# Optimization experiments

Measured on AMD Instinct MI355X. Metric: run time of the kernel, lower is better.

Reference implementation:

```python
import jax, jax.numpy as jnp
import numpy as np

N_NODES = 100000
D = 128
N_EDGES = 500000
HIDDEN = 256
NUM_CLASSES = 32


def setup_inputs() -> dict:
    key = jax.random.key(0)
    k0, k1, k2, k3 = jax.random.split(key, 4)
    node_embeddings = jax.random.normal(k0, (N_NODES, D), dtype=jnp.float32)
    edge_index = jax.random.randint(k1, (2, N_EDGES), 0, N_NODES, dtype=jnp.int64)
    # Linear weights in torch layout: [out_features, in_features]
    W1 = jax.random.normal(k2, (HIDDEN, 2 * D), dtype=jnp.float32) * (1.0 / np.sqrt(2 * D))
    b1 = jnp.zeros((HIDDEN,), dtype=jnp.float32)
    W2 = jax.random.normal(k3, (NUM_CLASSES, HIDDEN), dtype=jnp.float32) * (1.0 / np.sqrt(HIDDEN))
    b2 = jnp.zeros((NUM_CLASSES,), dtype=jnp.float32)
    return {"node_embeddings": node_embeddings, "edge_index": edge_index,
            "W1": W1, "b1": b1, "W2": W2, "b2": b2}


def reference(node_embeddings, edge_index, W1, b1, W2, b2):
    h = node_embeddings[edge_index[0]]            # [E, D]
    t = node_embeddings[edge_index[1]]            # [E, D]
    edge_emb = jnp.concatenate([h, t], axis=1)    # [E, 2D]
    out = edge_emb @ W1.T + b1                    # [E, HIDDEN]
    out = jax.nn.relu(out)
    out = out @ W2.T + b2                         # [E, NUM_CLASSES]
    return out
```

## Files before the change

kernel.cpp:

```cpp
#include <hip/hip_runtime.h>

constexpr int D    = 128;
constexpr int K2   = 256;
constexpr int H    = 256;
constexpr int CLS  = 32;
constexpr int MT   = 64;
constexpr int LSTR = 264;

typedef __attribute__((ext_vector_type(8))) __bf16 bf16x8;
typedef __attribute__((ext_vector_type(8))) unsigned short ushort8;
typedef __attribute__((ext_vector_type(4))) float f32x4;

static __device__ __forceinline__ unsigned short f2b(float f) {
  unsigned int u = __float_as_uint(f);
  u += 0x7FFFu + ((u >> 16) & 1u);
  return (unsigned short)(u >> 16);
}

static __device__ __forceinline__ void gld_lds16(const unsigned short* gp, unsigned short* lp) {
  __builtin_amdgcn_global_load_lds(
      (const __attribute__((address_space(1))) void*)gp,
      (__attribute__((address_space(3))) void*)lp, 16, 0, 0);
}

__global__ void prep_weights(const float* __restrict__ W1, const float* __restrict__ W2,
                             const void* __restrict__ eidx,
                             unsigned short* __restrict__ W1b, unsigned short* __restrict__ W2b,
                             unsigned short* __restrict__ W2s,
                             int* __restrict__ flag64) {
  int i = blockIdx.x * 256 + threadIdx.x;
  if (i < H * K2)  W1b[i] = f2b(W1[i]);
  if (i < CLS * H) {
    unsigned short v = f2b(W2[i]);
    W2b[i] = v;
    int r = i >> 8, e = i & 255, g = e >> 3, j = e & 7;
    int slot = (g & 16) | ((g ^ (r & 15)) & 15);
    W2s[r * 256 + slot * 8 + j] = v;
  }
  if (blockIdx.x == 0 && threadIdx.x == 0) {
    const unsigned int* p = (const unsigned int*)eidx;
    int is64 = 1;
    for (int j = 0; j < 64; ++j) if (p[2 * j + 1] != 0u) { is64 = 0; break; }
    *flag64 = is64;
  }
}

__global__ void prep_table(const float* __restrict__ emb, unsigned short* __restrict__ tab, int n8) {
  int i = blockIdx.x * 256 + threadIdx.x;
  if (i < n8) {
    const float* gp = emb + (size_t)i * 8;
    f32x4 lo = *(const f32x4*)gp, hi = *(const f32x4*)(gp + 4);
    ushort8 v;
    v[0] = f2b(lo[0]); v[1] = f2b(lo[1]); v[2] = f2b(lo[2]); v[3] = f2b(lo[3]);
    v[4] = f2b(hi[0]); v[5] = f2b(hi[1]); v[6] = f2b(hi[2]); v[7] = f2b(hi[3]);
    *(ushort8*)(tab + (size_t)i * 8) = v;
  }
}

__global__ void prep_idx(const void* __restrict__ eidx, int* __restrict__ idx32, int n) {
  __shared__ int sflag;
  if (threadIdx.x == 0) {
    const unsigned int* p = (const unsigned int*)eidx;
    int is64 = 1;
    for (int j = 0; j < 64; ++j) if (p[2 * j + 1] != 0u) { is64 = 0; break; }
    sflag = is64;
  }
  __syncthreads();
  int j = blockIdx.x * 256 + threadIdx.x;
  if (j < n) idx32[j] = sflag ? (int)((const long long*)eidx)[j] : ((const int*)eidx)[j];
}

__global__ __launch_bounds__(256, 2)
void edge_mlp3(const unsigned short* __restrict__ tab, const int* __restrict__ idx32,
               const unsigned short* __restrict__ W1b, const unsigned short* __restrict__ W2s,
               const float* __restrict__ b1, const float* __restrict__ b2,
               float* __restrict__ out, int E, int ntiles) {
  __shared__ unsigned short Xs[2][MT * 256];
  __shared__ unsigned short W2l[CLS * 256];

  const int tid  = threadIdx.x;
  const int lane = tid & 63;
  const int w    = tid >> 6;
  const int l16  = lane & 15;
  const int q    = lane >> 4;

  bf16x8 afr[4][8];
  #pragma unroll
  for (int a = 0; a < 4; ++a) {
    const unsigned short* rp = W1b + (64 * w + 16 * a + l16) * K2 + q * 8;
    #pragma unroll
    for (int kk = 0; kk < 8; ++kk)
      afr[a][kk] = *(const bf16x8*)(rp + kk * 32);
  }
  f32x4 binit[4];
  #pragma unroll
  for (int a = 0; a < 4; ++a) binit[a] = *(const f32x4*)(b1 + 64 * w + 16 * a + 4 * q);
  f32x4 b2init[2];
  #pragma unroll
  for (int ct = 0; ct < 2; ++ct) b2init[ct] = *(const f32x4*)(b2 + 16 * ct + 4 * q);

  #pragma unroll
  for (int c = 0; c < 4; ++c) {
    const unsigned short* gp = W2s + (c * 256 + 64 * w + lane) * 8;
    unsigned short* lp = &W2l[(c * 256 + 64 * w) * 8];
    gld_lds16(gp, lp);
  }

  const int G    = lane & 31;
  const int half = G >> 4;
  const int sub  = lane >> 5;

  auto stage = [&](int t, int b) {
    #pragma unroll
    for (int c = 0; c < 8; ++c) {
      int mrow = 16 * w + 2 * c + sub;
      int e = t * MT + mrow; if (e >= E) e = E - 1;
      int id = idx32[half ? (E + e) : e];
      const unsigned short* gp = tab + (size_t)id * D + ((G ^ mrow) & 15) * 8;
      unsigned short* lp = &Xs[b][(16 * w + 2 * c) * 256];
      gld_lds16(gp, lp);
    }
  };

  int buf = 0;
  int t0 = blockIdx.x;
  if (t0 < ntiles) stage(t0, 0);
  asm volatile("s_waitcnt vmcnt(0)\n\ts_barrier" ::: "memory");

  for (int t = t0; t < ntiles; t += gridDim.x) {
    int tn = t + gridDim.x;
    if (tn < ntiles) stage(tn, buf ^ 1);
    __builtin_amdgcn_sched_barrier(0);

    f32x4 acc[4][4];
    #pragma unroll
    for (int a = 0; a < 4; ++a)
      #pragma unroll
      for (int tt = 0; tt < 4; ++tt) acc[a][tt] = binit[a];

    __builtin_amdgcn_s_setprio(1);
    #pragma unroll
    for (int tt = 0; tt < 4; ++tt) {
      const unsigned short* rowp = &Xs[buf][(16 * tt + l16) * 256];
      #pragma unroll
      for (int kk = 0; kk < 8; ++kk) {
        int slot = (4 * kk + q) ^ l16;
        bf16x8 bfrag = *(const bf16x8*)(rowp + slot * 8);
        #pragma unroll
        for (int a = 0; a < 4; ++a)
          acc[a][tt] = __builtin_amdgcn_mfma_f32_16x16x32_bf16(afr[a][kk], bfrag, acc[a][tt], 0, 0, 0);
      }
    }
    __builtin_amdgcn_s_setprio(0);
    asm volatile("s_barrier" ::: "memory");

    #pragma unroll
    for (int a = 0; a < 4; ++a) {
      int dg   = 8 * w + 2 * a + (q >> 1);
      int qodd = (q & 1) * 4;
      #pragma unroll
      for (int tt = 0; tt < 4; ++tt) {
        int m = 16 * tt + l16;
        f32x4 v = acc[a][tt];
        unsigned int p0 = (unsigned int)f2b(fmaxf(v[0], 0.f)) | ((unsigned int)f2b(fmaxf(v[1], 0.f)) << 16);
        unsigned int p1 = (unsigned int)f2b(fmaxf(v[2], 0.f)) | ((unsigned int)f2b(fmaxf(v[3], 0.f)) << 16);
        int slot = (dg & 16) | ((dg ^ l16) & 15);
        uint2 pp; pp.x = p0; pp.y = p1;
        *(uint2*)(&Xs[buf][m * 256 + slot * 8 + qodd]) = pp;
      }
    }
    asm volatile("s_waitcnt lgkmcnt(0)\n\ts_barrier" ::: "memory");

    f32x4 acc2[2];
    acc2[0] = b2init[0]; acc2[1] = b2init[1];
    const int mrow = 16 * w + l16;
    const unsigned short* yrow = &Xs[buf][mrow * 256];
    #pragma unroll
    for (int kk = 0; kk < 8; ++kk) {
      int slot = (4 * kk + q) ^ l16;
      bf16x8 yfrag = *(const bf16x8*)(yrow + slot * 8);
      #pragma unroll
      for (int ct = 0; ct < 2; ++ct) {
        bf16x8 wf = *(const bf16x8*)(&W2l[(16 * ct + l16) * 256 + slot * 8]);
        acc2[ct] = __builtin_amdgcn_mfma_f32_16x16x32_bf16(wf, yfrag, acc2[ct], 0, 0, 0);
      }
    }
    int e = t * MT + mrow;
    if (e < E) {
      #pragma unroll
      for (int ct = 0; ct < 2; ++ct)
        __builtin_nontemporal_store(acc2[ct], (f32x4*)(out + (size_t)e * CLS + 16 * ct + 4 * q));
    }
    asm volatile("s_waitcnt vmcnt(2)\n\ts_barrier" ::: "memory");
    buf ^= 1;
  }
}

__global__ __launch_bounds__(256, 2)
void edge_mlp_v1(const float* __restrict__ emb, const void* __restrict__ eidx,
                 const unsigned short* __restrict__ W1b, const unsigned short* __restrict__ W2b,
                 const float* __restrict__ b1, const float* __restrict__ b2,
                 const int* __restrict__ flag64,
                 float* __restrict__ out, int E, int ntiles) {
  __shared__ unsigned short Xsp[MT * LSTR];
  const int tid  = threadIdx.x;
  const int lane = tid & 63;
  const int w    = tid >> 6;
  const int l16  = lane & 15;
  const int q    = lane >> 4;
  const int is64 = *flag64;

  bf16x8 afr[4][8];
  #pragma unroll
  for (int a = 0; a < 4; ++a) {
    const unsigned short* rp = W1b + (64 * w + 16 * a + l16) * K2 + q * 8;
    #pragma unroll
    for (int kk = 0; kk < 8; ++kk) afr[a][kk] = *(const bf16x8*)(rp + kk * 32);
  }
  f32x4 binit[4];
  #pragma unroll
  for (int a = 0; a < 4; ++a) binit[a] = *(const f32x4*)(b1 + 64 * w + 16 * a + 4 * q);
  f32x4 b2init[2];
  #pragma unroll
  for (int ct = 0; ct < 2; ++ct) b2init[ct] = *(const f32x4*)(b2 + 16 * ct + 4 * q);

  for (int t = blockIdx.x; t < ntiles; t += gridDim.x) {
    const int e0 = t * MT;
    #pragma unroll
    for (int c = 0; c < 8; ++c) {
      int chunk = tid + c * 256;
      int m = chunk >> 5, col8 = chunk & 31;
      int e = e0 + m; if (e >= E) e = E - 1;
      int iofs = (col8 < 16) ? e : (E + e);
      long long node = is64 ? ((const long long*)eidx)[iofs] : (long long)(((const int*)eidx)[iofs]);
      const float* gp = emb + (int)node * D + (col8 & 15) * 8;
      f32x4 lo = *(const f32x4*)gp, hi = *(const f32x4*)(gp + 4);
      ushort8 v;
      v[0] = f2b(lo[0]); v[1] = f2b(lo[1]); v[2] = f2b(lo[2]); v[3] = f2b(lo[3]);
      v[4] = f2b(hi[0]); v[5] = f2b(hi[1]); v[6] = f2b(hi[2]); v[7] = f2b(hi[3]);
      *(ushort8*)&Xsp[m * LSTR + col8 * 8] = v;
    }
    __syncthreads();
    f32x4 acc[4][4];
    #pragma unroll
    for (int a = 0; a < 4; ++a)
      #pragma unroll
      for (int tt = 0; tt < 4; ++tt) acc[a][tt] = binit[a];
    #pragma unroll
    for (int tt = 0; tt < 4; ++tt) {
      #pragma unroll
      for (int kk = 0; kk < 8; ++kk) {
        bf16x8 bfrag = *(const bf16x8*)&Xsp[(16 * tt + l16) * LSTR + kk * 32 + q * 8];
        #pragma unroll
        for (int a = 0; a < 4; ++a)
          acc[a][tt] = __builtin_amdgcn_mfma_f32_16x16x32_bf16(afr[a][kk], bfrag, acc[a][tt], 0, 0, 0);
      }
    }
    __syncthreads();
    #pragma unroll
    for (int a = 0; a < 4; ++a) {
      int n0 = 64 * w + 16 * a + 4 * q;
      #pragma unroll
      for (int tt = 0; tt < 4; ++tt) {
        f32x4 v = acc[a][tt];
        unsigned int p0 = (unsigned int)f2b(fmaxf(v[0], 0.f)) | ((unsigned int)f2b(fmaxf(v[1], 0.f)) << 16);
        unsigned int p1 = (unsigned int)f2b(fmaxf(v[2], 0.f)) | ((unsigned int)f2b(fmaxf(v[3], 0.f)) << 16);
        uint2 pp; pp.x = p0; pp.y = p1;
        *(uint2*)&Xsp[(16 * tt + l16) * LSTR + n0] = pp;
      }
    }
    __syncthreads();
    f32x4 acc2[2];
    acc2[0] = b2init[0]; acc2[1] = b2init[1];
    const int mrow = 16 * w + l16;
    #pragma unroll
    for (int kk = 0; kk < 8; ++kk) {
      bf16x8 yfrag = *(const bf16x8*)&Xsp[mrow * LSTR + kk * 32 + q * 8];
      #pragma unroll
      for (int ct = 0; ct < 2; ++ct) {
        bf16x8 wf = *(const bf16x8*)(W2b + (16 * ct + l16) * H + kk * 32 + q * 8);
        acc2[ct] = __builtin_amdgcn_mfma_f32_16x16x32_bf16(wf, yfrag, acc2[ct], 0, 0, 0);
      }
    }
    int e = e0 + mrow;
    if (e < E) {
      #pragma unroll
      for (int ct = 0; ct < 2; ++ct)
        *(f32x4*)(out + (size_t)e * CLS + 16 * ct + 4 * q) = acc2[ct];
    }
    __syncthreads();
  }
}

__global__ void edge_mlp_naive(const float* __restrict__ emb, const void* __restrict__ eidx,
                               const float* __restrict__ W1, const float* __restrict__ b1,
                               const float* __restrict__ W2, const float* __restrict__ b2,
                               float* __restrict__ out, int E) {
  __shared__ float x[K2];
  __shared__ float y[H];
  __shared__ int flag;
  int e = blockIdx.x;
  if (threadIdx.x == 0) {
    const unsigned int* p = (const unsigned int*)eidx;
    int is64 = 1;
    for (int j = 0; j < 16; ++j) if (p[2 * j + 1] != 0u) { is64 = 0; break; }
    flag = is64;
  }
  __syncthreads();
  int tid = threadIdx.x;
  long long s, d;
  if (flag) { s = ((const long long*)eidx)[e]; d = ((const long long*)eidx)[E + e]; }
  else      { s = ((const int*)eidx)[e];       d = ((const int*)eidx)[E + e]; }
  if (tid < D) { x[tid] = emb[(int)s * D + tid]; x[D + tid] = emb[(int)d * D + tid]; }
  __syncthreads();
  float acc = b1[tid];
  const float* wr = W1 + tid * K2;
  for (int k = 0; k < K2; ++k) acc += x[k] * wr[k];
  y[tid] = fmaxf(acc, 0.f);
  __syncthreads();
  if (tid < CLS) {
    float a2 = b2[tid];
    const float* w2 = W2 + tid * H;
    for (int k = 0; k < H; ++k) a2 += y[k] * w2[k];
    out[(size_t)e * CLS + tid] = a2;
  }
}

extern "C" void kernel_launch(void* const* d_in, const int* in_sizes, int n_in,
                              void* d_out, int out_size, void* d_ws, size_t ws_size,
                              hipStream_t stream) {
  const float* emb  = (const float*)d_in[0];
  const void*  eidx = d_in[1];
  const float* W1   = (const float*)d_in[2];
  const float* b1   = (const float*)d_in[3];
  const float* W2   = (const float*)d_in[4];
  const float* b2   = (const float*)d_in[5];
  float* out = (float*)d_out;
  const int nodes_elems = in_sizes[0];
  const int E = in_sizes[1] / 2;
  const int ntiles = (E + MT - 1) / MT;

  size_t off_tab  = 0;
  size_t off_w1   = (off_tab + (size_t)nodes_elems * 2 + 15) & ~(size_t)15;
  size_t off_w2   = off_w1 + (size_t)H * K2 * 2;
  size_t off_w2s  = off_w2 + (size_t)CLS * H * 2;
  size_t off_idx  = (off_w2s + (size_t)CLS * H * 2 + 15) & ~(size_t)15;
  size_t off_flag = off_idx + (size_t)2 * E * 4;
  size_t need_full    = off_flag + 16;
  size_t need_weights = (size_t)(H * K2 + CLS * H) * 2 + 64;

  if (ws_size >= need_full) {
    unsigned short* tab   = (unsigned short*)((char*)d_ws + off_tab);
    unsigned short* W1b   = (unsigned short*)((char*)d_ws + off_w1);
    unsigned short* W2b   = (unsigned short*)((char*)d_ws + off_w2);
    unsigned short* W2s   = (unsigned short*)((char*)d_ws + off_w2s);
    int*            idx32 = (int*)((char*)d_ws + off_idx);
    int*            flag  = (int*)((char*)d_ws + off_flag);

    prep_weights<<<(H * K2 + 255) / 256, 256, 0, stream>>>(W1, W2, eidx, W1b, W2b, W2s, flag);
    prep_table<<<(nodes_elems / 8 + 255) / 256, 256, 0, stream>>>(emb, tab, nodes_elems / 8);
    prep_idx<<<(2 * E + 255) / 256, 256, 0, stream>>>(eidx, idx32, 2 * E);
    edge_mlp3<<<512, 256, 0, stream>>>(tab, idx32, W1b, W2s, b1, b2, out, E, ntiles);
  } else if (ws_size >= need_weights) {
    unsigned short* W1b = (unsigned short*)d_ws;
    unsigned short* W2b = W1b + H * K2;
    int* flag = (int*)(W2b + CLS * H);
    prep_weights<<<(H * K2 + 255) / 256, 256, 0, stream>>>(W1, W2, eidx, W1b, W2b, W2b, flag);
    edge_mlp_v1<<<1024, 256, 0, stream>>>(emb, eidx, W1b, W2b, b1, b2, flag, out, E, ntiles);
  } else {
    edge_mlp_naive<<<E, H, 0, stream>>>(emb, eidx, W1, b1, W2, b2, out, E);
  }
}
```

Measured before the change: 220.7 us.

## Split edge MLP work across 8 waves per block to halve per-wave registers

The fused edge-MLP kernel now runs 512 threads (8 waves) per block instead of 256. Each wave holds half as many W1 fragments and accumulators, stages half as many gathered rows, and computes one class tile of the second layer. This cuts per-wave register pressure and raises the wave count available to hide gather latency. In exchange, each block is synchronised more tightly, since the same 64-row tile is now shared by twice as many waves at every barrier. The launch bound asks for 4 blocks per CU, but LDS use of about 80 KB per block may cap residency below that.

```diff
diff --git a/kernel.cpp b/kernel.cpp
--- a/kernel.cpp
+++ b/kernel.cpp
@@ -70,8 +70,8 @@
   if (j < n) idx32[j] = sflag ? (int)((const long long*)eidx)[j] : ((const int*)eidx)[j];
 }
 
-__global__ __launch_bounds__(256, 2)
-void edge_mlp3(const unsigned short* __restrict__ tab, const int* __restrict__ idx32,
+__global__ __launch_bounds__(512, 4)
+void edge_mlp4(const unsigned short* __restrict__ tab, const int* __restrict__ idx32,
                const unsigned short* __restrict__ W1b, const unsigned short* __restrict__ W2s,
                const float* __restrict__ b1, const float* __restrict__ b2,
                float* __restrict__ out, int E, int ntiles) {
@@ -84,25 +84,25 @@
   const int l16  = lane & 15;
   const int q    = lane >> 4;
 
-  bf16x8 afr[4][8];
-  #pragma unroll
-  for (int a = 0; a < 4; ++a) {
-    const unsigned short* rp = W1b + (64 * w + 16 * a + l16) * K2 + q * 8;
+  bf16x8 afr[2][8];
+  #pragma unroll
+  for (int a = 0; a < 2; ++a) {
+    const unsigned short* rp = W1b + (32 * w + 16 * a + l16) * K2 + q * 8;
     #pragma unroll
     for (int kk = 0; kk < 8; ++kk)
       afr[a][kk] = *(const bf16x8*)(rp + kk * 32);
   }
-  f32x4 binit[4];
-  #pragma unroll
-  for (int a = 0; a < 4; ++a) binit[a] = *(const f32x4*)(b1 + 64 * w + 16 * a + 4 * q);
-  f32x4 b2init[2];
-  #pragma unroll
-  for (int ct = 0; ct < 2; ++ct) b2init[ct] = *(const f32x4*)(b2 + 16 * ct + 4 * q);
-
-  #pragma unroll
-  for (int c = 0; c < 4; ++c) {
-    const unsigned short* gp = W2s + (c * 256 + 64 * w + lane) * 8;
-    unsigned short* lp = &W2l[(c * 256 + 64 * w) * 8];
+  f32x4 binit[2];
+  #pragma unroll
+  for (int a = 0; a < 2; ++a) binit[a] = *(const f32x4*)(b1 + 32 * w + 16 * a + 4 * q);
+  const int ct  = w & 1;
+  const int wg  = w >> 1;
+  f32x4 b2init = *(const f32x4*)(b2 + 16 * ct + 4 * q);
+
+  #pragma unroll
+  for (int c = 0; c < 2; ++c) {
+    const unsigned short* gp = W2s + ((2 * w + c) * 64 + lane) * 8;
+    unsigned short* lp = &W2l[(2 * w + c) * 64 * 8];
     gld_lds16(gp, lp);
   }
 
@@ -112,12 +112,12 @@
 
   auto stage = [&](int t, int b) {
     #pragma unroll
-    for (int c = 0; c < 8; ++c) {
-      int mrow = 16 * w + 2 * c + sub;
+    for (int c = 0; c < 4; ++c) {
+      int mrow = 8 * w + 2 * c + sub;
       int e = t * MT + mrow; if (e >= E) e = E - 1;
       int id = idx32[half ? (E + e) : e];
       const unsigned short* gp = tab + (size_t)id * D + ((G ^ mrow) & 15) * 8;
-      unsigned short* lp = &Xs[b][(16 * w + 2 * c) * 256];
+      unsigned short* lp = &Xs[b][(8 * w + 2 * c) * 256];
       gld_lds16(gp, lp);
     }
   };
@@ -132,9 +132,9 @@
     if (tn < ntiles) stage(tn, buf ^ 1);
     __builtin_amdgcn_sched_barrier(0);
 
-    f32x4 acc[4][4];
-    #pragma unroll
-    for (int a = 0; a < 4; ++a)
+    f32x4 acc[2][4];
+    #pragma unroll
+    for (int a = 0; a < 2; ++a)
       #pragma unroll
       for (int tt = 0; tt < 4; ++tt) acc[a][tt] = binit[a];
 
@@ -147,7 +147,7 @@
         int slot = (4 * kk + q) ^ l16;
         bf16x8 bfrag = *(const bf16x8*)(rowp + slot * 8);
         #pragma unroll
-        for (int a = 0; a < 4; ++a)
+        for (int a = 0; a < 2; ++a)
           acc[a][tt] = __builtin_amdgcn_mfma_f32_16x16x32_bf16(afr[a][kk], bfrag, acc[a][tt], 0, 0, 0);
       }
     }
@@ -155,8 +155,8 @@
     asm volatile("s_barrier" ::: "memory");
 
     #pragma unroll
-    for (int a = 0; a < 4; ++a) {
-      int dg   = 8 * w + 2 * a + (q >> 1);
+    for (int a = 0; a < 2; ++a) {
+      int dg   = 4 * w + 2 * a + (q >> 1);
       int qodd = (q & 1) * 4;
       #pragma unroll
       for (int tt = 0; tt < 4; ++tt) {
@@ -171,27 +171,20 @@
     }
     asm volatile("s_waitcnt lgkmcnt(0)\n\ts_barrier" ::: "memory");
 
-    f32x4 acc2[2];
-    acc2[0] = b2init[0]; acc2[1] = b2init[1];
-    const int mrow = 16 * w + l16;
+    f32x4 acc2 = b2init;
+    const int mrow = 16 * wg + l16;
     const unsigned short* yrow = &Xs[buf][mrow * 256];
     #pragma unroll
     for (int kk = 0; kk < 8; ++kk) {
       int slot = (4 * kk + q) ^ l16;
       bf16x8 yfrag = *(const bf16x8*)(yrow + slot * 8);
-      #pragma unroll
-      for (int ct = 0; ct < 2; ++ct) {
-        bf16x8 wf = *(const bf16x8*)(&W2l[(16 * ct + l16) * 256 + slot * 8]);
-        acc2[ct] = __builtin_amdgcn_mfma_f32_16x16x32_bf16(wf, yfrag, acc2[ct], 0, 0, 0);
-      }
+      bf16x8 wf = *(const bf16x8*)(&W2l[(16 * ct + l16) * 256 + slot * 8]);
+      acc2 = __builtin_amdgcn_mfma_f32_16x16x32_bf16(wf, yfrag, acc2, 0, 0, 0);
     }
     int e = t * MT + mrow;
-    if (e < E) {
-      #pragma unroll
-      for (int ct = 0; ct < 2; ++ct)
-        __builtin_nontemporal_store(acc2[ct], (f32x4*)(out + (size_t)e * CLS + 16 * ct + 4 * q));
-    }
-    asm volatile("s_waitcnt vmcnt(2)\n\ts_barrier" ::: "memory");
+    if (e < E)
+      __builtin_nontemporal_store(acc2, (f32x4*)(out + (size_t)e * CLS + 16 * ct + 4 * q));
+    asm volatile("s_waitcnt vmcnt(1)\n\ts_barrier" ::: "memory");
     buf ^= 1;
   }
 }
@@ -360,7 +353,7 @@
     prep_weights<<<(H * K2 + 255) / 256, 256, 0, stream>>>(W1, W2, eidx, W1b, W2b, W2s, flag);
     prep_table<<<(nodes_elems / 8 + 255) / 256, 256, 0, stream>>>(emb, tab, nodes_elems / 8);
     prep_idx<<<(2 * E + 255) / 256, 256, 0, stream>>>(eidx, idx32, 2 * E);
-    edge_mlp3<<<512, 256, 0, stream>>>(tab, idx32, W1b, W2s, b1, b2, out, E, ntiles);
+    edge_mlp4<<<512, 512, 0, stream>>>(tab, idx32, W1b, W2s, b1, b2, out, E, ntiles);
   } else if (ws_size >= need_weights) {
     unsigned short* W1b = (unsigned short*)d_ws;
     unsigned short* W2b = W1b + H * K2;
```

Result: slower. 292.4 us (+32.5%).

## Bucket-sort edges by head node to improve gather locality

Applied to the files above, without the earlier changes.

Adds a histogram, scan and scatter pass that groups edges by head-node index (bins of 8 nodes), then runs a new MLP kernel over the sorted edges and writes results back through a permutation. The goal is for head-node embedding gathers to hit in cache more often. In exchange it adds three extra kernel launches, global atomics, extra index traffic and scattered output stores. The tail-node gathers stay random.

```diff
diff --git a/kernel.cpp b/kernel.cpp
--- a/kernel.cpp
+++ b/kernel.cpp
@@ -6,6 +6,7 @@
 constexpr int CLS  = 32;
 constexpr int MT   = 64;
 constexpr int LSTR = 264;
+constexpr int NBINS = 16384;
 
 typedef __attribute__((ext_vector_type(8))) __bf16 bf16x8;
 typedef __attribute__((ext_vector_type(8))) unsigned short ushort8;
@@ -27,9 +28,11 @@
                              const void* __restrict__ eidx,
                              unsigned short* __restrict__ W1b, unsigned short* __restrict__ W2b,
                              unsigned short* __restrict__ W2s,
+                             int* __restrict__ hist,
                              int* __restrict__ flag64) {
   int i = blockIdx.x * 256 + threadIdx.x;
   if (i < H * K2)  W1b[i] = f2b(W1[i]);
+  if (hist && i < NBINS) hist[i] = 0;
   if (i < CLS * H) {
     unsigned short v = f2b(W2[i]);
     W2b[i] = v;
@@ -57,7 +60,8 @@
   }
 }
 
-__global__ void prep_idx(const void* __restrict__ eidx, int* __restrict__ idx32, int n) {
+__global__ void prep_idx_hist(const void* __restrict__ eidx, int* __restrict__ idx32,
+                              int* __restrict__ hist, int E) {
   __shared__ int sflag;
   if (threadIdx.x == 0) {
     const unsigned int* p = (const unsigned int*)eidx;
@@ -67,7 +71,179 @@
   }
   __syncthreads();
   int j = blockIdx.x * 256 + threadIdx.x;
-  if (j < n) idx32[j] = sflag ? (int)((const long long*)eidx)[j] : ((const int*)eidx)[j];
+  if (j < 2 * E) {
+    int v = sflag ? (int)((const long long*)eidx)[j] : ((const int*)eidx)[j];
+    idx32[j] = v;
+    if (hist && j < E) atomicAdd(&hist[min(v >> 3, NBINS - 1)], 1);
+  }
+}
+
+__global__ __launch_bounds__(1024)
+void scan_bins(const int* __restrict__ hist, int* __restrict__ offs) {
+  __shared__ int ps[1024];
+  const int tIdx = threadIdx.x;
+  const int b0 = tIdx * (NBINS / 1024);
+  int s = 0;
+  #pragma unroll
+  for (int i = 0; i < NBINS / 1024; ++i) s += hist[b0 + i];
+  ps[tIdx] = s;
+  __syncthreads();
+  for (int off = 1; off < 1024; off <<= 1) {
+    int v = (tIdx >= off) ? ps[tIdx - off] : 0;
+    __syncthreads();
+    ps[tIdx] += v;
+    __syncthreads();
+  }
+  int run = ps[tIdx] - s;
+  #pragma unroll
+  for (int i = 0; i < NBINS / 1024; ++i) { int h = hist[b0 + i]; offs[b0 + i] = run; run += h; }
+}
+
+__global__ void scatter_edges(const int* __restrict__ idx32, int* __restrict__ offs,
+                              int* __restrict__ sidx, int* __restrict__ perm, int E) {
+  int j = blockIdx.x * 256 + threadIdx.x;
+  if (j < E) {
+    int h = idx32[j];
+    int pos = atomicAdd(&offs[min(h >> 3, NBINS - 1)], 1);
+    sidx[pos]     = h;
+    sidx[E + pos] = idx32[E + j];
+    perm[pos]     = j;
+  }
+}
+
+__global__ __launch_bounds__(256, 2)
+void edge_mlp5(const unsigned short* __restrict__ tab, const int* __restrict__ sidx,
+               const int* __restrict__ perm,
+               const unsigned short* __restrict__ W1b, const unsigned short* __restrict__ W2s,
+               const float* __restrict__ b1, const float* __restrict__ b2,
+               float* __restrict__ out, int E, int ntiles) {
+  __shared__ unsigned short Xs[2][MT * 256];
+  __shared__ unsigned short W2l[CLS * 256];
+
+  const int tid  = threadIdx.x;
+  const int lane = tid & 63;
+  const int w    = tid >> 6;
+  const int l16  = lane & 15;
+  const int q    = lane >> 4;
+
+  bf16x8 afr[4][8];
+  #pragma unroll
+  for (int a = 0; a < 4; ++a) {
+    const unsigned short* rp = W1b + (64 * w + 16 * a + l16) * K2 + q * 8;
+    #pragma unroll
+    for (int kk = 0; kk < 8; ++kk)
+      afr[a][kk] = *(const bf16x8*)(rp + kk * 32);
+  }
+  f32x4 binit[4];
+  #pragma unroll
+  for (int a = 0; a < 4; ++a) binit[a] = *(const f32x4*)(b1 + 64 * w + 16 * a + 4 * q);
+  f32x4 b2init[2];
+  #pragma unroll
+  for (int ct = 0; ct < 2; ++ct) b2init[ct] = *(const f32x4*)(b2 + 16 * ct + 4 * q);
+
+  #pragma unroll
+  for (int c = 0; c < 4; ++c) {
+    const unsigned short* gp = W2s + (c * 256 + 64 * w + lane) * 8;
+    unsigned short* lp = &W2l[(c * 256 + 64 * w) * 8];
+    gld_lds16(gp, lp);
+  }
+
+  const int G    = lane & 31;
+  const int half = G >> 4;
+  const int sub  = lane >> 5;
+
+  auto stage = [&](int t, int b) {
+    #pragma unroll
+    for (int c = 0; c < 8; ++c) {
+      int mrow = 16 * w + 2 * c + sub;
+      int e = t * MT + mrow; if (e >= E) e = E - 1;
+      int id = sidx[half ? (E + e) : e];
+      const unsigned short* gp = tab + (size_t)id * D + ((G ^ mrow) & 15) * 8;
+      unsigned short* lp = &Xs[b][(16 * w + 2 * c) * 256];
+      gld_lds16(gp, lp);
+    }
+  };
+
+  const int nbk  = gridDim.x;
+  const int cid  = (blockIdx.x & 7) * (nbk >> 3) + (blockIdx.x >> 3);
+  const int base = ntiles / nbk, ext = ntiles % nbk;
+  const int tstart = cid * base + min(cid, ext);
+  const int tend   = tstart + base + (cid < ext ? 1 : 0);
+
+  int buf = 0;
+  if (tstart < tend) stage(tstart, 0);
+  asm volatile("s_waitcnt vmcnt(0)\n\ts_barrier" ::: "memory");
+
+  const int mrow_st = 16 * w + l16;
+  for (int t = tstart; t < tend; ++t) {
+    int e_s = t * MT + mrow_st;
+    int pe = 0;
+    if (e_s < E) pe = perm[e_s];
+
+    int tn = t + 1;
+    if (tn < tend) stage(tn, buf ^ 1);
+    __builtin_amdgcn_sched_barrier(0);
+
+    f32x4 acc[4][4];
+    #pragma unroll
+    for (int a = 0; a < 4; ++a)
+      #pragma unroll
+      for (int tt = 0; tt < 4; ++tt) acc[a][tt] = binit[a];
+
+    __builtin_amdgcn_s_setprio(1);
+    #pragma unroll
+    for (int tt = 0; tt < 4; ++tt) {
+      const unsigned short* rowp = &Xs[buf][(16 * tt + l16) * 256];
+      #pragma unroll
+      for (int kk = 0; kk < 8; ++kk) {
+        int slot = (4 * kk + q) ^ l16;
+        bf16x8 bfrag = *(const bf16x8*)(rowp + slot * 8);
+        #pragma unroll
+        for (int a = 0; a < 4; ++a)
+          acc[a][tt] = __builtin_amdgcn_mfma_f32_16x16x32_bf16(afr[a][kk], bfrag, acc[a][tt], 0, 0, 0);
+      }
+    }
+    __builtin_amdgcn_s_setprio(0);
+    asm volatile("s_barrier" ::: "memory");
+
+    #pragma unroll
+    for (int a = 0; a < 4; ++a) {
+      int dg   = 8 * w + 2 * a + (q >> 1);
+      int qodd = (q & 1) * 4;
+      #pragma unroll
+      for (int tt = 0; tt < 4; ++tt) {
+        int m = 16 * tt + l16;
+        f32x4 v = acc[a][tt];
+        unsigned int p0 = (unsigned int)f2b(fmaxf(v[0], 0.f)) | ((unsigned int)f2b(fmaxf(v[1], 0.f)) << 16);
+        unsigned int p1 = (unsigned int)f2b(fmaxf(v[2], 0.f)) | ((unsigned int)f2b(fmaxf(v[3], 0.f)) << 16);
+        int slot = (dg & 16) | ((dg ^ l16) & 15);
+        uint2 pp; pp.x = p0; pp.y = p1;
+        *(uint2*)(&Xs[buf][m * 256 + slot * 8 + qodd]) = pp;
+      }
+    }
+    asm volatile("s_waitcnt lgkmcnt(0)\n\ts_barrier" ::: "memory");
+
+    f32x4 acc2[2];
+    acc2[0] = b2init[0]; acc2[1] = b2init[1];
+    const unsigned short* yrow = &Xs[buf][mrow_st * 256];
+    #pragma unroll
+    for (int kk = 0; kk < 8; ++kk) {
+      int slot = (4 * kk + q) ^ l16;
+      bf16x8 yfrag = *(const bf16x8*)(yrow + slot * 8);
+      #pragma unroll
+      for (int ct = 0; ct < 2; ++ct) {
+        bf16x8 wf = *(const bf16x8*)(&W2l[(16 * ct + l16) * 256 + slot * 8]);
+        acc2[ct] = __builtin_amdgcn_mfma_f32_16x16x32_bf16(wf, yfrag, acc2[ct], 0, 0, 0);
+      }
+    }
+    if (e_s < E) {
+      #pragma unroll
+      for (int ct = 0; ct < 2; ++ct)
+        __builtin_nontemporal_store(acc2[ct], (f32x4*)(out + (size_t)pe * CLS + 16 * ct + 4 * q));
+    }
+    asm volatile("s_waitcnt vmcnt(2)\n\ts_barrier" ::: "memory");
+    buf ^= 1;
+  }
 }
 
 __global__ __launch_bounds__(256, 2)
@@ -345,27 +521,49 @@
   size_t off_w2   = off_w1 + (size_t)H * K2 * 2;
   size_t off_w2s  = off_w2 + (size_t)CLS * H * 2;
   size_t off_idx  = (off_w2s + (size_t)CLS * H * 2 + 15) & ~(size_t)15;
-  size_t off_flag = off_idx + (size_t)2 * E * 4;
-  size_t need_full    = off_flag + 16;
+  size_t off_sidx = off_idx + (size_t)2 * E * 4;
+  size_t off_perm = off_sidx + (size_t)2 * E * 4;
+  size_t off_hist = off_perm + (size_t)E * 4;
+  size_t off_offs = off_hist + (size_t)NBINS * 4;
+  size_t off_flag = off_offs + (size_t)NBINS * 4;
+  size_t need_sort    = off_flag + 16;
+  size_t need_v3      = off_sidx + 16;
   size_t need_weights = (size_t)(H * K2 + CLS * H) * 2 + 64;
 
-  if (ws_size >= need_full) {
+  if (ws_size >= need_sort) {
     unsigned short* tab   = (unsigned short*)((char*)d_ws + off_tab);
     unsigned short* W1b   = (unsigned short*)((char*)d_ws + off_w1);
     unsigned short* W2b   = (unsigned short*)((char*)d_ws + off_w2);
     unsigned short* W2s   = (unsigned short*)((char*)d_ws + off_w2s);
     int*            idx32 = (int*)((char*)d_ws + off_idx);
+    int*            sidx  = (int*)((char*)d_ws + off_sidx);
+    int*            perm  = (int*)((char*)d_ws + off_perm);
+    int*            hist  = (int*)((char*)d_ws + off_hist);
+    int*            offs  = (int*)((char*)d_ws + off_offs);
     int*            flag  = (int*)((char*)d_ws + off_flag);
 
-    prep_weights<<<(H * K2 + 255) / 256, 256, 0, stream>>>(W1, W2, eidx, W1b, W2b, W2s, flag);
+    prep_weights<<<(H * K2 + 255) / 256, 256, 0, stream>>>(W1, W2, eidx, W1b, W2b, W2s, hist, flag);
     prep_table<<<(nodes_elems / 8 + 255) / 256, 256, 0, stream>>>(emb, tab, nodes_elems / 8);
-    prep_idx<<<(2 * E + 255) / 256, 256, 0, stream>>>(eidx, idx32, 2 * E);
+    prep_idx_hist<<<(2 * E + 255) / 256, 256, 0, stream>>>(eidx, idx32, hist, E);
+    scan_bins<<<1, 1024, 0, stream>>>(hist, offs);
+    scatter_edges<<<(E + 255) / 256, 256, 0, stream>>>(idx32, offs, sidx, perm, E);
+    edge_mlp5<<<512, 256, 0, stream>>>(tab, sidx, perm, W1b, W2s, b1, b2, out, E, ntiles);
+  } else if (ws_size >= need_v3) {
+    unsigned short* tab   = (unsigned short*)((char*)d_ws + off_tab);
+    unsigned short* W1b   = (unsigned short*)((char*)d_ws + off_w1);
+    unsigned short* W2b   = (unsigned short*)((char*)d_ws + off_w2);
+    unsigned short* W2s   = (unsigned short*)((char*)d_ws + off_w2s);
+    int*            idx32 = (int*)((char*)d_ws + off_idx);
+    int*            flag  = (int*)((char*)d_ws + off_sidx);
+    prep_weights<<<(H * K2 + 255) / 256, 256, 0, stream>>>(W1, W2, eidx, W1b, W2b, W2s, (int*)0, flag);
+    prep_table<<<(nodes_elems / 8 + 255) / 256, 256, 0, stream>>>(emb, tab, nodes_elems / 8);
+    prep_idx_hist<<<(2 * E + 255) / 256, 256, 0, stream>>>(eidx, idx32, (int*)0, E);
     edge_mlp3<<<512, 256, 0, stream>>>(tab, idx32, W1b, W2s, b1, b2, out, E, ntiles);
   } else if (ws_size >= need_weights) {
     unsigned short* W1b = (unsigned short*)d_ws;
     unsigned short* W2b = W1b + H * K2;
     int* flag = (int*)(W2b + CLS * H);
-    prep_weights<<<(H * K2 + 255) / 256, 256, 0, stream>>>(W1, W2, eidx, W1b, W2b, W2b, flag);
+    prep_weights<<<(H * K2 + 255) / 256, 256, 0, stream>>>(W1, W2, eidx, W1b, W2b, W2b, (int*)0, flag);
     edge_mlp_v1<<<1024, 256, 0, stream>>>(emb, eidx, W1b, W2b, b1, b2, flag, out, E, ntiles);
   } else {
     edge_mlp_naive<<<E, H, 0, stream>>>(emb, eidx, W1, b1, W2, b2, out, E);
```

Result: slower. 296.0 us (+34.1%).
